# Kernel optimization log

Hardware: AMD Instinct MI355X
Metric: run time of the kernel (lower is better)

## Reference

```python
import jax, jax.numpy as jnp
import numpy as np

B, N, C, DP, H, P = 1, 768, 384, 128, 12, 4
HP3 = H * P * 3


def setup_inputs() -> dict:
    key = jax.random.key(0)
    ks = jax.random.split(key, 16)
    w = lambda k, shp: (jax.random.normal(k, shp, jnp.float32) * 0.02)
    inp = {
        'single': jax.random.normal(ks[0], (B, N, C), jnp.float32),
        'pair': jax.random.normal(ks[1], (B, N, N, DP), jnp.float32),
        'rot': jax.random.normal(ks[2], (B, N, 3, 3), jnp.float32),
        'trans': jax.random.normal(ks[3], (B, N, 3), jnp.float32),
        'q_w': w(ks[4], (C, C)), 'q_b': jnp.zeros((C,), jnp.float32),
        'k_w': w(ks[5], (C, C)), 'k_b': jnp.zeros((C,), jnp.float32),
        'v_w': w(ks[6], (C, C)), 'v_b': jnp.zeros((C,), jnp.float32),
        'pb_w': w(ks[7], (H, DP)), 'pb_b': jnp.zeros((H,), jnp.float32),
        'qp_w': w(ks[8], (HP3, C)), 'qp_b': jnp.zeros((HP3,), jnp.float32),
        'kp_w': w(ks[9], (HP3, C)), 'kp_b': jnp.zeros((HP3,), jnp.float32),
        'vp_w': w(ks[10], (HP3, C)), 'vp_b': jnp.zeros((HP3,), jnp.float32),
        'pt_w': w(ks[11], (C, HP3)), 'pt_b': jnp.zeros((C,), jnp.float32),
        'out_w': w(ks[12], (C, C)), 'out_b': jnp.zeros((C,), jnp.float32),
        'ln_g': jnp.ones((C,), jnp.float32), 'ln_b': jnp.zeros((C,), jnp.float32),
    }
    return inp


def _lin(x, w, b):
    return x @ w.T + b


def reference(single, pair, rot, trans, q_w, q_b, k_w, k_b, v_w, v_b,
              pb_w, pb_b, qp_w, qp_b, kp_w, kp_b, vp_w, vp_b,
              pt_w, pt_b, out_w, out_b, ln_g, ln_b):
    Bs, Ns, Cs = single.shape
    Ch = Cs // H
    scale = Ch ** (-0.5)

    q = _lin(single, q_w, q_b).reshape(Bs, Ns, H, Ch)
    k = _lin(single, k_w, k_b).reshape(Bs, Ns, H, Ch)
    v = _lin(single, v_w, v_b).reshape(Bs, Ns, H, Ch)

    pair_bias = jnp.transpose(_lin(pair, pb_w, pb_b), (0, 3, 1, 2))  # b h i j

    def to_global(w_, b_):
        pts = _lin(single, w_, b_).reshape(Bs, Ns, H, P, 3)
        return jnp.einsum('bnhpi,bnij->bnhpj', pts, rot) + trans[:, :, None, None, :]

    qg = to_global(qp_w, qp_b)
    kg = to_global(kp_w, kp_b)

    q2 = jnp.sum(qg * qg, axis=(3, 4))  # b n h
    k2 = jnp.sum(kg * kg, axis=(3, 4))
    qk = jnp.einsum('bihpd,bjhpd->bijh', qg, kg)
    point_logits = -0.5 * (q2[:, :, None, :] + k2[:, None, :, :] - 2.0 * qk)  # b i j h
    point_logits = jnp.transpose(point_logits, (0, 3, 1, 2)) * scale  # b h i j

    scalar_logits = jnp.einsum('bnhc,bmhc->bhnm', q, k) * scale
    attn = jax.nn.softmax(scalar_logits + pair_bias + point_logits, axis=-1)

    weighted = jnp.einsum('bhnm,bmhc->bnhc', attn, v).reshape(Bs, Ns, Cs)

    vg = to_global(vp_w, vp_b)
    point_weighted = jnp.einsum('bhnm,bmhpd->bnhpd', attn, vg).reshape(Bs, Ns, HP3)
    point_proj = _lin(point_weighted, pt_w, pt_b)

    out = _lin(weighted + point_proj, out_w, out_b)
    x = single + out
    mu = jnp.mean(x, axis=-1, keepdims=True)
    var = jnp.var(x, axis=-1, keepdims=True)
    return (x - mu) / jnp.sqrt(var + 1e-5) * ln_g + ln_b
```

## Files before the change

### kernel.cpp

```cpp
#include <hip/hip_runtime.h>
#include <hip/hip_bf16.h>
#include <cstddef>

#define NN 768
#define CC 384
#define HH 12
#define DPP 128
#define OFF_Q   0
#define OFF_K   294912
#define OFF_V   589824
#define OFF_QP  884736
#define OFF_KP  995328
#define OFF_VP  1105920
#define OFF_WTD 1216512
#define OFF_PW  1511424
#define OFF_LOG 1622016

__global__ __launch_bounds__(256) void k_proj(
    const float* __restrict__ single,
    const float* __restrict__ qw, const float* __restrict__ qb,
    const float* __restrict__ kw, const float* __restrict__ kb,
    const float* __restrict__ vw, const float* __restrict__ vb,
    const float* __restrict__ qpw, const float* __restrict__ qpb,
    const float* __restrict__ kpw, const float* __restrict__ kpb,
    const float* __restrict__ vpw, const float* __restrict__ vpb,
    float* __restrict__ ws)
{
    __shared__ float As[64][33];
    __shared__ float Bs[48][33];
    const int tid = threadIdx.x;
    const int i0 = blockIdx.y * 64;
    const int n0 = blockIdx.x * 48;
    const int tx = tid & 15, ty = tid >> 4;
    float acc[4][3] = {};
    for (int k0 = 0; k0 < CC; k0 += 32) {
        #pragma unroll
        for (int l = tid; l < 64 * 32; l += 256) {
            int r = l >> 5, c = l & 31;
            As[r][c] = single[(size_t)(i0 + r) * CC + k0 + c];
        }
        #pragma unroll
        for (int l = tid; l < 48 * 32; l += 256) {
            int r = l >> 5, c = l & 31;
            int n = n0 + r;
            const float* wp; int row;
            if (n < 1152) { int m = n / CC; row = n - m * CC; wp = (m == 0) ? qw : ((m == 1) ? kw : vw); }
            else { int np = n - 1152; int m = np / 144; row = np - m * 144; wp = (m == 0) ? qpw : ((m == 1) ? kpw : vpw); }
            Bs[r][c] = wp[(size_t)row * CC + k0 + c];
        }
        __syncthreads();
        #pragma unroll
        for (int kk = 0; kk < 32; ++kk) {
            float av[4], bv[3];
            #pragma unroll
            for (int a = 0; a < 4; ++a) av[a] = As[ty * 4 + a][kk];
            #pragma unroll
            for (int b = 0; b < 3; ++b) bv[b] = Bs[tx * 3 + b][kk];
            #pragma unroll
            for (int a = 0; a < 4; ++a)
                #pragma unroll
                for (int b = 0; b < 3; ++b)
                    acc[a][b] = fmaf(av[a], bv[b], acc[a][b]);
        }
        __syncthreads();
    }
    #pragma unroll
    for (int a = 0; a < 4; ++a) {
        int i = i0 + ty * 4 + a;
        #pragma unroll
        for (int b = 0; b < 3; ++b) {
            int n = n0 + tx * 3 + b;
            float bias; size_t dst;
            if (n < 1152) {
                int m = n / CC; int c = n - m * CC;
                bias = ((m == 0) ? qb : ((m == 1) ? kb : vb))[c];
                dst = (size_t)m * 294912 + (size_t)i * CC + c;
            } else {
                int np = n - 1152; int m = np / 144; int c = np - m * 144;
                bias = ((m == 0) ? qpb : ((m == 1) ? kpb : vpb))[c];
                dst = (size_t)OFF_QP + (size_t)m * 110592 + (size_t)i * 144 + c;
            }
            ws[dst] = acc[a][b] + bias;
        }
    }
}

__global__ __launch_bounds__(256) void k_to_global(
    const float* __restrict__ rot, const float* __restrict__ trans, float* __restrict__ ws)
{
    int id = blockIdx.x * 256 + threadIdx.x;
    if (id >= 3 * NN * 48) return;
    int t3 = id / (NN * 48);
    int rem = id - t3 * (NN * 48);
    int n = rem / 48;
    int hp = rem - n * 48;
    float* arr = ws + OFF_QP + (size_t)t3 * 110592 + (size_t)n * 144 + hp * 3;
    float p0 = arr[0], p1 = arr[1], p2 = arr[2];
    const float* R = rot + (size_t)n * 9;
    const float* T = trans + (size_t)n * 3;
    arr[0] = p0 * R[0] + p1 * R[3] + p2 * R[6] + T[0];
    arr[1] = p0 * R[1] + p1 * R[4] + p2 * R[7] + T[1];
    arr[2] = p0 * R[2] + p1 * R[5] + p2 * R[8] + T[2];
}

__global__ __launch_bounds__(256) void k_pairbias(
    const float* __restrict__ pair,
    const float* __restrict__ pbw, const float* __restrict__ pbb,
    float* __restrict__ logits)
{
    const int tid = threadIdx.x;
    const int i = blockIdx.x;
    const int j = blockIdx.y * 256 + tid;

    float acc[12];
    #pragma unroll
    for (int h = 0; h < HH; ++h) acc[h] = pbb[h];

    const float4* pr = (const float4*)(pair + ((size_t)i * NN + j) * DPP);
    const float4* w4 = (const float4*)pbw;

    #pragma unroll 4
    for (int k4 = 0; k4 < 32; ++k4) {
        float4 p = pr[k4];
        #pragma unroll
        for (int h = 0; h < HH; ++h) {
            float4 w = w4[h * 32 + k4];
            acc[h] = fmaf(p.x, w.x, acc[h]);
            acc[h] = fmaf(p.y, w.y, acc[h]);
            acc[h] = fmaf(p.z, w.z, acc[h]);
            acc[h] = fmaf(p.w, w.w, acc[h]);
        }
    }
    #pragma unroll
    for (int h = 0; h < HH; ++h)
        logits[((size_t)h * NN + i) * NN + j] = acc[h];
}

__global__ __launch_bounds__(256) void k_qk(
    const float* __restrict__ q, const float* __restrict__ k,
    const float* __restrict__ qg, const float* __restrict__ kg,
    float* __restrict__ logits)
{
    const float scale = 0.17677669529663687f;
    const int tid = threadIdx.x;
    const int i0 = blockIdx.x * 48;
    const int jc = blockIdx.y;
    const int h  = blockIdx.z;
    const int j  = jc * 256 + tid;

    float kf[32];
    const float4* kp4 = (const float4*)(k + (size_t)j * CC + h * 32);
    #pragma unroll
    for (int t = 0; t < 8; ++t) {
        float4 tv = kp4[t];
        kf[4 * t + 0] = tv.x; kf[4 * t + 1] = tv.y; kf[4 * t + 2] = tv.z; kf[4 * t + 3] = tv.w;
    }
    float kgf[12];
    const float4* kg4 = (const float4*)(kg + (size_t)j * 144 + h * 12);
    #pragma unroll
    for (int t = 0; t < 3; ++t) {
        float4 tv = kg4[t];
        kgf[4 * t + 0] = tv.x; kgf[4 * t + 1] = tv.y; kgf[4 * t + 2] = tv.z; kgf[4 * t + 3] = tv.w;
    }

    #pragma unroll 4
    for (int ii = 0; ii < 48; ++ii) {
        const int i = i0 + ii;
        size_t idx = ((size_t)h * NN + i) * NN + j;
        float old = logits[idx];
        const float* qrow = q + (size_t)i * CC + h * 32;
        float dt = 0.f;
        #pragma unroll
        for (int c = 0; c < 32; ++c) dt = fmaf(kf[c], qrow[c], dt);
        const float* qgrow = qg + (size_t)i * 144 + h * 12;
        float pt = 0.f;
        #pragma unroll
        for (int e = 0; e < 12; ++e) { float d2 = qgrow[e] - kgf[e]; pt = fmaf(d2, d2, pt); }
        logits[idx] = old + scale * dt - 0.5f * scale * pt;
    }
}

__global__ __launch_bounds__(256) void k_soft(
    const float* __restrict__ logits, const float* __restrict__ v, const float* __restrict__ vg,
    float* __restrict__ weighted, float* __restrict__ pw)
{
    __shared__ float att[8][772];
    __shared__ float vt[128][45];
    const int tid = threadIdx.x;
    const int h = blockIdx.y;
    const int i0 = blockIdx.x * 8;

    for (int idx = tid; idx < 8 * 192; idx += 256) {
        int r = idx / 192, c4 = idx - r * 192;
        float4 tv = ((const float4*)(logits + ((size_t)h * NN + i0 + r) * NN))[c4];
        float* dp = &att[r][c4 * 4];
        dp[0] = tv.x; dp[1] = tv.y; dp[2] = tv.z; dp[3] = tv.w;
    }
    __syncthreads();
    {
        int r = tid >> 5, lane = tid & 31;
        float m = -1e30f;
        for (int jj = lane; jj < NN; jj += 32) m = fmaxf(m, att[r][jj]);
        #pragma unroll
        for (int off = 16; off; off >>= 1) m = fmaxf(m, __shfl_xor(m, off, 32));
        float s = 0.f;
        for (int jj = lane; jj < NN; jj += 32) { float e = __expf(att[r][jj] - m); att[r][jj] = e; s += e; }
        #pragma unroll
        for (int off = 16; off; off >>= 1) s += __shfl_xor(s, off, 32);
        float inv = 1.f / s;
        for (int jj = lane; jj < NN; jj += 32) att[r][jj] *= inv;
    }
    __syncthreads();

    float acc0 = 0.f, acc1 = 0.f;
    const int o0 = tid, o1 = tid + 256;
    const int r0 = o0 / 44, d0 = o0 - r0 * 44;
    const int o1c = (o1 < 352) ? o1 : 351;
    const int r1 = o1c / 44, d1 = o1c - r1 * 44;
    for (int jc = 0; jc < 6; ++jc) {
        for (int idx = tid; idx < 128 * 44; idx += 256) {
            int jj = idx / 44, d = idx - jj * 44;
            int jg = jc * 128 + jj;
            vt[jj][d] = (d < 32) ? v[(size_t)jg * CC + h * 32 + d]
                                 : vg[(size_t)jg * 144 + h * 12 + (d - 32)];
        }
        __syncthreads();
        const float* a0p = &att[r0][jc * 128];
        const float* a1p = &att[r1][jc * 128];
        #pragma unroll 4
        for (int jj = 0; jj < 128; ++jj) {
            acc0 = fmaf(a0p[jj], vt[jj][d0], acc0);
            acc1 = fmaf(a1p[jj], vt[jj][d1], acc1);
        }
        __syncthreads();
    }
    {
        int i = i0 + r0;
        if (d0 < 32) weighted[(size_t)i * CC + h * 32 + d0] = acc0;
        else         pw[(size_t)i * 144 + h * 12 + (d0 - 32)] = acc0;
    }
    if (o1 < 352) {
        int i = i0 + r1;
        if (d1 < 32) weighted[(size_t)i * CC + h * 32 + d1] = acc1;
        else         pw[(size_t)i * 144 + h * 12 + (d1 - 32)] = acc1;
    }
}

__global__ __launch_bounds__(384) void k_out(
    const float* __restrict__ single,
    const float* __restrict__ weighted, const float* __restrict__ pwv,
    const float* __restrict__ ptw, const float* __restrict__ ptb,
    const float* __restrict__ outw, const float* __restrict__ outb,
    const float* __restrict__ lng, const float* __restrict__ lnb,
    float* __restrict__ out)
{
    __shared__ float pw_s[4][144];
    __shared__ float tmp_s[4][388];
    __shared__ float red[16];
    const int tid = threadIdx.x;
    const int i0 = blockIdx.x * 4;
    for (int idx = tid; idx < 4 * 144; idx += 384) {
        int r = idx / 144, e = idx - r * 144;
        pw_s[r][e] = pwv[(size_t)(i0 + r) * 144 + e];
    }
    __syncthreads();
    const int c = tid;
    float t[4];
    {
        float a[4] = {0.f, 0.f, 0.f, 0.f};
        const float4* wp4 = (const float4*)(ptw + (size_t)c * 144);
        #pragma unroll 4
        for (int e4 = 0; e4 < 36; ++e4) {
            float4 w4 = wp4[e4];
            #pragma unroll
            for (int r = 0; r < 4; ++r) {
                float4 pv = *(const float4*)&pw_s[r][e4 * 4];
                a[r] = fmaf(w4.x, pv.x, a[r]);
                a[r] = fmaf(w4.y, pv.y, a[r]);
                a[r] = fmaf(w4.z, pv.z, a[r]);
                a[r] = fmaf(w4.w, pv.w, a[r]);
            }
        }
        float pb = ptb[c];
        #pragma unroll
        for (int r = 0; r < 4; ++r)
            t[r] = weighted[(size_t)(i0 + r) * CC + c] + pb + a[r];
    }
    #pragma unroll
    for (int r = 0; r < 4; ++r) tmp_s[r][c] = t[r];
    __syncthreads();
    float o[4];
    {
        float ob = outb[c];
        #pragma unroll
        for (int r = 0; r < 4; ++r) o[r] = ob;
        const float4* wp4 = (const float4*)(outw + (size_t)c * CC);
        #pragma unroll 2
        for (int e4 = 0; e4 < 96; ++e4) {
            float4 w4 = wp4[e4];
            #pragma unroll
            for (int r = 0; r < 4; ++r) {
                float4 tv = *(const float4*)&tmp_s[r][e4 * 4];
                o[r] = fmaf(w4.x, tv.x, o[r]);
                o[r] = fmaf(w4.y, tv.y, o[r]);
                o[r] = fmaf(w4.z, tv.z, o[r]);
                o[r] = fmaf(w4.w, tv.w, o[r]);
            }
        }
        #pragma unroll
        for (int r = 0; r < 4; ++r) o[r] += single[(size_t)(i0 + r) * CC + c];
    }
    float g = lng[c], bb = lnb[c];
    #pragma unroll
    for (int rr = 0; rr < 4; ++rr) {
        float xs = o[rr], xq = o[rr] * o[rr];
        #pragma unroll
        for (int off = 32; off; off >>= 1) {
            xs += __shfl_xor(xs, off, 64);
            xq += __shfl_xor(xq, off, 64);
        }
        __syncthreads();
        if ((tid & 63) == 0) { int w = tid >> 6; red[w] = xs; red[8 + w] = xq; }
        __syncthreads();
        float S = red[0] + red[1] + red[2] + red[3] + red[4] + red[5];
        float Q = red[8] + red[9] + red[10] + red[11] + red[12] + red[13];
        float mu = S * (1.f / 384.f);
        float var = Q * (1.f / 384.f) - mu * mu;
        float rs = rsqrtf(var + 1e-5f);
        out[(size_t)(i0 + rr) * CC + c] = (o[rr] - mu) * rs * g + bb;
    }
}

extern "C" void kernel_launch(void* const* d_in, const int* in_sizes, int n_in,
                              void* d_out, int out_size, void* d_ws, size_t ws_size,
                              hipStream_t stream)
{
    const float* single = (const float*)d_in[0];
    const float* pair   = (const float*)d_in[1];
    const float* rot    = (const float*)d_in[2];
    const float* trans  = (const float*)d_in[3];
    const float* qw  = (const float*)d_in[4];  const float* qb  = (const float*)d_in[5];
    const float* kw  = (const float*)d_in[6];  const float* kb  = (const float*)d_in[7];
    const float* vw  = (const float*)d_in[8];  const float* vb  = (const float*)d_in[9];
    const float* pbw = (const float*)d_in[10]; const float* pbb = (const float*)d_in[11];
    const float* qpw = (const float*)d_in[12]; const float* qpb = (const float*)d_in[13];
    const float* kpw = (const float*)d_in[14]; const float* kpb = (const float*)d_in[15];
    const float* vpw = (const float*)d_in[16]; const float* vpb = (const float*)d_in[17];
    const float* ptw = (const float*)d_in[18]; const float* ptb = (const float*)d_in[19];
    const float* outw = (const float*)d_in[20]; const float* outb = (const float*)d_in[21];
    const float* lng  = (const float*)d_in[22]; const float* lnb  = (const float*)d_in[23];

    float* ws = (float*)d_ws;
    float* q   = ws + OFF_Q;
    float* k   = ws + OFF_K;
    float* v   = ws + OFF_V;
    float* qg  = ws + OFF_QP;
    float* kg  = ws + OFF_KP;
    float* vg  = ws + OFF_VP;
    float* wtd = ws + OFF_WTD;
    float* pwv = ws + OFF_PW;
    float* logits = ws + OFF_LOG;

    dim3 g1(33, 12);
    hipLaunchKernelGGL(k_proj, g1, dim3(256), 0, stream,
                       single, qw, qb, kw, kb, vw, vb, qpw, qpb, kpw, kpb, vpw, vpb, ws);
    hipLaunchKernelGGL(k_to_global, dim3(432), dim3(256), 0, stream, rot, trans, ws);
    dim3 g3a(768, 3);
    hipLaunchKernelGGL(k_pairbias, g3a, dim3(256), 0, stream, pair, pbw, pbb, logits);
    dim3 g3b(16, 3, 12);
    hipLaunchKernelGGL(k_qk, g3b, dim3(256), 0, stream, q, k, qg, kg, logits);
    dim3 g4(96, 12);
    hipLaunchKernelGGL(k_soft, g4, dim3(256), 0, stream, logits, v, vg, wtd, pwv);
    hipLaunchKernelGGL(k_out, dim3(192), dim3(384), 0, stream,
                       single, wtd, pwv, ptw, ptb, outw, outb, lng, lnb, (float*)d_out);
}
```

Before: 378.3 us.

## Coalesce pair loads via LDS staging, vectorize proj LDS reads, one row per k_out block

```diff
diff --git a/kernel.cpp b/kernel.cpp
--- a/kernel.cpp
+++ b/kernel.cpp
@@ -26,8 +26,8 @@
     const float* __restrict__ vpw, const float* __restrict__ vpb,
     float* __restrict__ ws)
 {
-    __shared__ float As[64][33];
-    __shared__ float Bs[48][33];
+    __shared__ float As[64][36];
+    __shared__ float Bs[48][36];
     const int tid = threadIdx.x;
     const int i0 = blockIdx.y * 64;
     const int n0 = blockIdx.x * 48;
@@ -50,17 +50,21 @@
         }
         __syncthreads();
         #pragma unroll
-        for (int kk = 0; kk < 32; ++kk) {
-            float av[4], bv[3];
-            #pragma unroll
-            for (int a = 0; a < 4; ++a) av[a] = As[ty * 4 + a][kk];
-            #pragma unroll
-            for (int b = 0; b < 3; ++b) bv[b] = Bs[tx * 3 + b][kk];
+        for (int kk4 = 0; kk4 < 8; ++kk4) {
+            float4 av[4], bv[3];
+            #pragma unroll
+            for (int a = 0; a < 4; ++a) av[a] = *(const float4*)&As[ty * 4 + a][kk4 * 4];
+            #pragma unroll
+            for (int b = 0; b < 3; ++b) bv[b] = *(const float4*)&Bs[tx * 3 + b][kk4 * 4];
             #pragma unroll
             for (int a = 0; a < 4; ++a)
                 #pragma unroll
-                for (int b = 0; b < 3; ++b)
-                    acc[a][b] = fmaf(av[a], bv[b], acc[a][b]);
+                for (int b = 0; b < 3; ++b) {
+                    acc[a][b] = fmaf(av[a].x, bv[b].x, acc[a][b]);
+                    acc[a][b] = fmaf(av[a].y, bv[b].y, acc[a][b]);
+                    acc[a][b] = fmaf(av[a].z, bv[b].z, acc[a][b]);
+                    acc[a][b] = fmaf(av[a].w, bv[b].w, acc[a][b]);
+                }
         }
         __syncthreads();
     }
@@ -108,32 +112,58 @@
     const float* __restrict__ pbw, const float* __restrict__ pbb,
     float* __restrict__ logits)
 {
+    __shared__ float sp[256][33];
     const int tid = threadIdx.x;
     const int i = blockIdx.x;
-    const int j = blockIdx.y * 256 + tid;
+    const int j0 = blockIdx.y * 256;
+    const float4* w4 = (const float4*)pbw;
 
     float acc[12];
     #pragma unroll
     for (int h = 0; h < HH; ++h) acc[h] = pbb[h];
 
-    const float4* pr = (const float4*)(pair + ((size_t)i * NN + j) * DPP);
-    const float4* w4 = (const float4*)pbw;
-
-    #pragma unroll 4
-    for (int k4 = 0; k4 < 32; ++k4) {
-        float4 p = pr[k4];
-        #pragma unroll
-        for (int h = 0; h < HH; ++h) {
-            float4 w = w4[h * 32 + k4];
-            acc[h] = fmaf(p.x, w.x, acc[h]);
-            acc[h] = fmaf(p.y, w.y, acc[h]);
-            acc[h] = fmaf(p.z, w.z, acc[h]);
-            acc[h] = fmaf(p.w, w.w, acc[h]);
-        }
+    const int lrow = tid >> 3;
+    const int lcol = tid & 7;
+    const float* pbase = pair + ((size_t)i * NN + j0) * DPP;
+
+    float4 st[8];
+    #pragma unroll
+    for (int p = 0; p < 8; ++p) {
+        int row = p * 32 + lrow;
+        st[p] = *(const float4*)(pbase + (size_t)row * DPP + lcol * 4);
+    }
+
+    for (int cc = 0; cc < 4; ++cc) {
+        #pragma unroll
+        for (int p = 0; p < 8; ++p) {
+            int row = p * 32 + lrow;
+            *(float4*)&sp[row][lcol * 4] = st[p];
+        }
+        __syncthreads();
+        if (cc < 3) {
+            #pragma unroll
+            for (int p = 0; p < 8; ++p) {
+                int row = p * 32 + lrow;
+                st[p] = *(const float4*)(pbase + (size_t)row * DPP + (cc + 1) * 32 + lcol * 4);
+            }
+        }
+        #pragma unroll
+        for (int c4 = 0; c4 < 8; ++c4) {
+            float4 pv = *(const float4*)&sp[tid][c4 * 4];
+            #pragma unroll
+            for (int h = 0; h < HH; ++h) {
+                float4 w = w4[h * 32 + cc * 8 + c4];
+                acc[h] = fmaf(pv.x, w.x, acc[h]);
+                acc[h] = fmaf(pv.y, w.y, acc[h]);
+                acc[h] = fmaf(pv.z, w.z, acc[h]);
+                acc[h] = fmaf(pv.w, w.w, acc[h]);
+            }
+        }
+        __syncthreads();
     }
     #pragma unroll
     for (int h = 0; h < HH; ++h)
-        logits[((size_t)h * NN + i) * NN + j] = acc[h];
+        logits[((size_t)h * NN + i) * NN + j0 + tid] = acc[h];
 }
 
 __global__ __launch_bounds__(256) void k_qk(
@@ -254,81 +284,57 @@
     const float* __restrict__ lng, const float* __restrict__ lnb,
     float* __restrict__ out)
 {
-    __shared__ float pw_s[4][144];
-    __shared__ float tmp_s[4][388];
-    __shared__ float red[16];
-    const int tid = threadIdx.x;
-    const int i0 = blockIdx.x * 4;
-    for (int idx = tid; idx < 4 * 144; idx += 384) {
-        int r = idx / 144, e = idx - r * 144;
-        pw_s[r][e] = pwv[(size_t)(i0 + r) * 144 + e];
-    }
+    __shared__ float pw_s[144];
+    __shared__ float tmp_s[384];
+    __shared__ float red[12];
+    const int tid = threadIdx.x;
+    const int i = blockIdx.x;
+    if (tid < 144) pw_s[tid] = pwv[(size_t)i * 144 + tid];
     __syncthreads();
     const int c = tid;
-    float t[4];
+    float a = 0.f;
     {
-        float a[4] = {0.f, 0.f, 0.f, 0.f};
         const float4* wp4 = (const float4*)(ptw + (size_t)c * 144);
         #pragma unroll 4
         for (int e4 = 0; e4 < 36; ++e4) {
             float4 w4 = wp4[e4];
-            #pragma unroll
-            for (int r = 0; r < 4; ++r) {
-                float4 pv = *(const float4*)&pw_s[r][e4 * 4];
-                a[r] = fmaf(w4.x, pv.x, a[r]);
-                a[r] = fmaf(w4.y, pv.y, a[r]);
-                a[r] = fmaf(w4.z, pv.z, a[r]);
-                a[r] = fmaf(w4.w, pv.w, a[r]);
-            }
-        }
-        float pb = ptb[c];
-        #pragma unroll
-        for (int r = 0; r < 4; ++r)
-            t[r] = weighted[(size_t)(i0 + r) * CC + c] + pb + a[r];
-    }
-    #pragma unroll
-    for (int r = 0; r < 4; ++r) tmp_s[r][c] = t[r];
-    __syncthreads();
-    float o[4];
+            float4 pv = *(const float4*)&pw_s[e4 * 4];
+            a = fmaf(w4.x, pv.x, a);
+            a = fmaf(w4.y, pv.y, a);
+            a = fmaf(w4.z, pv.z, a);
+            a = fmaf(w4.w, pv.w, a);
+        }
+    }
+    tmp_s[c] = weighted[(size_t)i * CC + c] + ptb[c] + a;
+    __syncthreads();
+    float o = outb[c];
     {
-        float ob = outb[c];
-        #pragma unroll
-        for (int r = 0; r < 4; ++r) o[r] = ob;
         const float4* wp4 = (const float4*)(outw + (size_t)c * CC);
         #pragma unroll 2
         for (int e4 = 0; e4 < 96; ++e4) {
             float4 w4 = wp4[e4];
-            #pragma unroll
-            for (int r = 0; r < 4; ++r) {
-                float4 tv = *(const float4*)&tmp_s[r][e4 * 4];
-                o[r] = fmaf(w4.x, tv.x, o[r]);
-                o[r] = fmaf(w4.y, tv.y, o[r]);
-                o[r] = fmaf(w4.z, tv.z, o[r]);
-                o[r] = fmaf(w4.w, tv.w, o[r]);
-            }
-        }
-        #pragma unroll
-        for (int r = 0; r < 4; ++r) o[r] += single[(size_t)(i0 + r) * CC + c];
-    }
-    float g = lng[c], bb = lnb[c];
-    #pragma unroll
-    for (int rr = 0; rr < 4; ++rr) {
-        float xs = o[rr], xq = o[rr] * o[rr];
-        #pragma unroll
-        for (int off = 32; off; off >>= 1) {
-            xs += __shfl_xor(xs, off, 64);
-            xq += __shfl_xor(xq, off, 64);
-        }
-        __syncthreads();
-        if ((tid & 63) == 0) { int w = tid >> 6; red[w] = xs; red[8 + w] = xq; }
-        __syncthreads();
-        float S = red[0] + red[1] + red[2] + red[3] + red[4] + red[5];
-        float Q = red[8] + red[9] + red[10] + red[11] + red[12] + red[13];
-        float mu = S * (1.f / 384.f);
-        float var = Q * (1.f / 384.f) - mu * mu;
-        float rs = rsqrtf(var + 1e-5f);
-        out[(size_t)(i0 + rr) * CC + c] = (o[rr] - mu) * rs * g + bb;
-    }
+            float4 tv = *(const float4*)&tmp_s[e4 * 4];
+            o = fmaf(w4.x, tv.x, o);
+            o = fmaf(w4.y, tv.y, o);
+            o = fmaf(w4.z, tv.z, o);
+            o = fmaf(w4.w, tv.w, o);
+        }
+    }
+    o += single[(size_t)i * CC + c];
+    float xs = o, xq = o * o;
+    #pragma unroll
+    for (int off = 32; off; off >>= 1) {
+        xs += __shfl_xor(xs, off, 64);
+        xq += __shfl_xor(xq, off, 64);
+    }
+    if ((tid & 63) == 0) { int w = tid >> 6; red[w] = xs; red[6 + w] = xq; }
+    __syncthreads();
+    float S = red[0] + red[1] + red[2] + red[3] + red[4] + red[5];
+    float Q = red[6] + red[7] + red[8] + red[9] + red[10] + red[11];
+    float mu = S * (1.f / 384.f);
+    float var = Q * (1.f / 384.f) - mu * mu;
+    float rs = rsqrtf(var + 1e-5f);
+    out[(size_t)i * CC + c] = (o - mu) * rs * lng[c] + lnb[c];
 }
 
 extern "C" void kernel_launch(void* const* d_in, const int* in_sizes, int n_in,
@@ -365,12 +371,12 @@
     hipLaunchKernelGGL(k_proj, g1, dim3(256), 0, stream,
                        single, qw, qb, kw, kb, vw, vb, qpw, qpb, kpw, kpb, vpw, vpb, ws);
     hipLaunchKernelGGL(k_to_global, dim3(432), dim3(256), 0, stream, rot, trans, ws);
-    dim3 g3a(768, 3);
-    hipLaunchKernelGGL(k_pairbias, g3a, dim3(256), 0, stream, pair, pbw, pbb, logits);
+    dim3 g3(768, 3);
+    hipLaunchKernelGGL(k_pairbias, g3, dim3(256), 0, stream, pair, pbw, pbb, logits);
     dim3 g3b(16, 3, 12);
     hipLaunchKernelGGL(k_qk, g3b, dim3(256), 0, stream, q, k, qg, kg, logits);
     dim3 g4(96, 12);
     hipLaunchKernelGGL(k_soft, g4, dim3(256), 0, stream, logits, v, vg, wtd, pwv);
-    hipLaunchKernelGGL(k_out, dim3(192), dim3(384), 0, stream,
+    hipLaunchKernelGGL(k_out, dim3(768), dim3(384), 0, stream,
                        single, wtd, pwv, ptw, ptb, outw, outb, lng, lnb, (float*)d_out);
 }
```

Result: slower. 422.3 us (+11.6%).
